# Kernel optimization log

Hardware: AMD Instinct MI355X
Metric: run time of the kernel (lower is better)

Reference implementation:

```python
import jax, jax.numpy as jnp
import numpy as np

A = 20.0  # sigmoid sharpness used by the module

def norm_sigmoid(x):
    # module's sigmoid: min/max normalize over the whole tensor, then steep sigmoid
    xn = (x - jnp.min(x)) / (jnp.max(x) - jnp.min(x))
    return jax.nn.sigmoid(A * xn)

def setup_inputs() -> dict:
    key = jax.random.key(0)
    ks = jax.random.split(key, 10)
    B, T = 2048, 512
    input_dim, nh1, nh2, nh3, output_dim = 1, 256, 256, 128, 1
    def lin(k, fan_in, fan_out):
        bound = 1.0 / np.sqrt(fan_in)
        kw, kb = jax.random.split(k)
        W = jax.random.uniform(kw, (fan_out, fan_in), jnp.float32, -bound, bound)
        b = jax.random.uniform(kb, (fan_out,), jnp.float32, -bound, bound)
        return W, b
    W1, b1 = lin(ks[0], input_dim, nh1)
    W2, b2 = lin(ks[1], nh1, nh2)
    W4, b4 = lin(ks[2], nh3, output_dim)
    j_w = jax.random.normal(ks[3], (nh3,), jnp.float32)
    k_w = jax.random.normal(ks[4], (nh3,), jnp.float32)
    X = jax.random.normal(ks[5], (B, T), jnp.float32)
    return {"X": X, "W1": W1, "b1": b1, "W2": W2, "b2": b2,
            "W4": W4, "b4": b4, "j_w": j_w, "k_w": k_w}

def reference(X, W1, b1, W2, b2, W4, b4, j_w, k_w):
    B, T = X.shape
    nh3 = j_w.shape[0]
    xs = jnp.swapaxes(X, 0, 1)[:, :, None]  # [T, B, 1] scalar input per step

    def step(state, x_t):
        out1 = norm_sigmoid(x_t @ W1.T + b1)          # [B, nh1]
        out2 = norm_sigmoid(out1 @ W2.T + b2)         # [B, nh2]
        j, k = out2[:, :nh3], out2[:, nh3:]
        inp_j = norm_sigmoid(j * j_w)
        inp_k = norm_sigmoid(k * k_w)
        new_state = (1.0 - state) * inp_j + (1.0 - inp_k) * state  # flip-flop update
        out4 = norm_sigmoid(new_state @ W4.T + b4)    # [B, 1]
        return new_state, out4

    state0 = jnp.zeros((B, nh3), X.dtype)
    _, ys = jax.lax.scan(step, state0, xs)            # ys: [T, B, 1]
    return jnp.squeeze(jnp.swapaxes(ys, 0, 1), axis=2)  # [B, T]
```

## Files before the change

### kernel.cpp

```cpp
#include <hip/hip_runtime.h>

#define TT 512
#define BB 2048
#define HH 256

typedef _Float16 f16x8 __attribute__((ext_vector_type(8)));
typedef _Float16 f16x4 __attribute__((ext_vector_type(4)));
typedef float f32x4 __attribute__((ext_vector_type(4)));

__device__ __forceinline__ float sigf(float z) { return 1.0f / (1.0f + __expf(-z)); }
__device__ __forceinline__ unsigned f2o(float f) {
    unsigned u = __float_as_uint(f);
    return (u & 0x80000000u) ? ~u : (u | 0x80000000u);
}
__device__ __forceinline__ float o2f(unsigned o) {
    unsigned u = (o & 0x80000000u) ? (o & 0x7fffffffu) : ~o;
    return __uint_as_float(u);
}

__global__ __launch_bounds__(256) void k0_stats(const float* __restrict__ X,
                                                const float* __restrict__ W1,
                                                const float* __restrict__ b1,
                                                float* __restrict__ mn1f, float* __restrict__ s1f,
                                                unsigned* __restrict__ colGmn,
                                                unsigned* __restrict__ colGmx,
                                                float2* __restrict__ statep) {
    int t = blockIdx.x, tid = threadIdx.x;
    statep[blockIdx.x * 256 + tid] = make_float2(0.f, 0.f);
    colGmn[(size_t)t * 256 + tid] = 0xFFFFFFFFu;
    colGmx[(size_t)t * 256 + tid] = 0u;
    __shared__ float rmn[256], rmx[256];
    float mn = 3.4e38f, mx = -3.4e38f;
    for (int b = tid; b < BB; b += 256) {
        float v = X[(size_t)b * TT + t];
        mn = fminf(mn, v); mx = fmaxf(mx, v);
    }
    rmn[tid] = mn; rmx[tid] = mx; __syncthreads();
    for (int s = 128; s > 0; s >>= 1) {
        if (tid < s) { rmn[tid] = fminf(rmn[tid], rmn[tid + s]); rmx[tid] = fmaxf(rmx[tid], rmx[tid + s]); }
        __syncthreads();
    }
    float xmn = rmn[0], xmx = rmx[0];
    __syncthreads();
    float w = W1[tid], bb = b1[tid];
    float v0 = w * xmn + bb, v1 = w * xmx + bb;
    rmn[tid] = fminf(v0, v1); rmx[tid] = fmaxf(v0, v1); __syncthreads();
    for (int s = 128; s > 0; s >>= 1) {
        if (tid < s) { rmn[tid] = fminf(rmn[tid], rmn[tid + s]); rmx[tid] = fmaxf(rmx[tid], rmx[tid + s]); }
        __syncthreads();
    }
    if (tid == 0) {
        mn1f[t] = rmn[0];
        s1f[t] = 20.0f / (rmx[0] - rmn[0]);
    }
}

__global__ __launch_bounds__(256) void k0b_cvt(const float* __restrict__ W2, _Float16* __restrict__ W2h) {
    int i4 = (blockIdx.x * 256 + threadIdx.x) * 4;
    float4 v = *(const float4*)&W2[i4];
    f16x4 h;
    h[0] = (_Float16)v.x; h[1] = (_Float16)v.y; h[2] = (_Float16)v.z; h[3] = (_Float16)v.w;
    *(f16x4*)&W2h[i4] = h;
}

__global__ __launch_bounds__(512) void k1_gemm(const float* __restrict__ X,
                                               const float* __restrict__ W1,
                                               const float* __restrict__ b1,
                                               const _Float16* __restrict__ W2h,
                                               const float* __restrict__ b2,
                                               const float* __restrict__ mn1f,
                                               const float* __restrict__ s1f,
                                               float* __restrict__ buf,
                                               unsigned* __restrict__ colGmn,
                                               unsigned* __restrict__ colGmx,
                                               int tbase) {
    int tl = blockIdx.z, t = tbase + tl;
    int bBase = blockIdx.x * 128;
    int tid = threadIdx.x;
    __shared__ __align__(16) _Float16 A_lds[128 * 72];
    __shared__ __align__(16) _Float16 B_lds[256 * 72];
    __shared__ float x_s[128];
    __shared__ unsigned cmnL[256], cmxL[256];
    if (tid < 128) x_s[tid] = X[(size_t)(bBase + tid) * TT + t];
    if (tid < 256) { cmnL[tid] = 0xFFFFFFFFu; cmxL[tid] = 0u; }
    float mn1 = mn1f[t], s1 = s1f[t];
    int lane = tid & 63, w = tid >> 6;
    int wr = w >> 2, wc = w & 3;
    int l15 = lane & 15, lk = (lane >> 4) * 8;
    f32x4 acc[4][4];
#pragma unroll
    for (int i = 0; i < 4; ++i)
#pragma unroll
        for (int j = 0; j < 4; ++j) acc[i][j] = (f32x4)0.0f;

    for (int kc = 0; kc < HH; kc += 64) {
        __syncthreads();
#pragma unroll
        for (int it = 0; it < 2; ++it) {
            int idx = it * 512 + tid;
            int row = idx >> 3, kg = (idx & 7) * 8;
            float x = x_s[row];
            float4 wa = *(const float4*)&W1[kc + kg];
            float4 wb = *(const float4*)&W1[kc + kg + 4];
            float4 ba = *(const float4*)&b1[kc + kg];
            float4 bb = *(const float4*)&b1[kc + kg + 4];
            f16x8 av;
            av[0] = (_Float16)sigf((x * wa.x + ba.x - mn1) * s1);
            av[1] = (_Float16)sigf((x * wa.y + ba.y - mn1) * s1);
            av[2] = (_Float16)sigf((x * wa.z + ba.z - mn1) * s1);
            av[3] = (_Float16)sigf((x * wa.w + ba.w - mn1) * s1);
            av[4] = (_Float16)sigf((x * wb.x + bb.x - mn1) * s1);
            av[5] = (_Float16)sigf((x * wb.y + bb.y - mn1) * s1);
            av[6] = (_Float16)sigf((x * wb.z + bb.z - mn1) * s1);
            av[7] = (_Float16)sigf((x * wb.w + bb.w - mn1) * s1);
            *(f16x8*)&A_lds[row * 72 + kg] = av;
        }
#pragma unroll
        for (int it = 0; it < 4; ++it) {
            int idx = it * 512 + tid;
            int c = idx >> 3, kg = (idx & 7) * 8;
            *(f16x8*)&B_lds[c * 72 + kg] = *(const f16x8*)&W2h[(size_t)c * HH + kc + kg];
        }
        __syncthreads();
#pragma unroll
        for (int ks = 0; ks < 64; ks += 32) {
            f16x8 af[4], bf[4];
#pragma unroll
            for (int i = 0; i < 4; ++i)
                af[i] = *(const f16x8*)&A_lds[(wr * 64 + i * 16 + l15) * 72 + ks + lk];
#pragma unroll
            for (int j = 0; j < 4; ++j)
                bf[j] = *(const f16x8*)&B_lds[(wc * 64 + j * 16 + l15) * 72 + ks + lk];
#pragma unroll
            for (int i = 0; i < 4; ++i)
#pragma unroll
                for (int j = 0; j < 4; ++j)
                    acc[i][j] = __builtin_amdgcn_mfma_f32_16x16x32_f16(af[i], bf[j], acc[i][j], 0, 0, 0);
        }
    }
#pragma unroll
    for (int j = 0; j < 4; ++j) {
        int c = wc * 64 + j * 16 + l15;
        float b2v = b2[c];
        float vmn = 3.4e38f, vmx = -3.4e38f;
#pragma unroll
        for (int i = 0; i < 4; ++i) {
            int r0 = wr * 64 + i * 16 + ((lane >> 4) << 2);
#pragma unroll
            for (int q = 0; q < 4; ++q) {
                float v = acc[i][j][q] + b2v;
                buf[((size_t)tl * BB + bBase + r0 + q) * HH + c] = v;
                vmn = fminf(vmn, v); vmx = fmaxf(vmx, v);
            }
        }
        atomicMin(&cmnL[c], f2o(vmn));
        atomicMax(&cmxL[c], f2o(vmx));
    }
    __syncthreads();
    if (tid < 256) {
        atomicMin(&colGmn[(size_t)t * 256 + tid], cmnL[tid]);
        atomicMax(&colGmx[(size_t)t * 256 + tid], cmxL[tid]);
    }
}

__global__ __launch_bounds__(256) void k1b(const unsigned* __restrict__ colGmn,
                                           const unsigned* __restrict__ colGmx,
                                           const float* __restrict__ j_w,
                                           const float* __restrict__ k_w,
                                           float* __restrict__ mn2f, float* __restrict__ s2f,
                                           float* __restrict__ mjf, float* __restrict__ sjf,
                                           float* __restrict__ mkf, float* __restrict__ skf,
                                           int tbase) {
    int t = tbase + blockIdx.x, tid = threadIdx.x;
    __shared__ float ra[256], rb[256];
    float cmn = o2f(colGmn[(size_t)t * 256 + tid]);
    float cmx = o2f(colGmx[(size_t)t * 256 + tid]);
    ra[tid] = cmn; rb[tid] = cmx; __syncthreads();
    for (int s = 128; s > 0; s >>= 1) {
        if (tid < s) { ra[tid] = fminf(ra[tid], ra[tid + s]); rb[tid] = fmaxf(rb[tid], rb[tid + s]); }
        __syncthreads();
    }
    float mn2 = ra[0], mx2 = rb[0];
    float s2 = 20.0f / (mx2 - mn2);
    __syncthreads();
    float lo = 3.4e38f, hi = -3.4e38f;
    if (tid < 128) {
        float wv = j_w[tid];
        float a = sigf((cmn - mn2) * s2) * wv;
        float b = sigf((cmx - mn2) * s2) * wv;
        lo = fminf(a, b); hi = fmaxf(a, b);
    }
    ra[tid] = lo; rb[tid] = hi; __syncthreads();
    for (int s = 128; s > 0; s >>= 1) {
        if (tid < s) { ra[tid] = fminf(ra[tid], ra[tid + s]); rb[tid] = fmaxf(rb[tid], rb[tid + s]); }
        __syncthreads();
    }
    float mj = ra[0], mxj = rb[0];
    __syncthreads();
    lo = 3.4e38f; hi = -3.4e38f;
    if (tid >= 128) {
        float wv = k_w[tid - 128];
        float a = sigf((cmn - mn2) * s2) * wv;
        float b = sigf((cmx - mn2) * s2) * wv;
        lo = fminf(a, b); hi = fmaxf(a, b);
    }
    ra[tid] = lo; rb[tid] = hi; __syncthreads();
    for (int s = 128; s > 0; s >>= 1) {
        if (tid < s) { ra[tid] = fminf(ra[tid], ra[tid + s]); rb[tid] = fmaxf(rb[tid], rb[tid + s]); }
        __syncthreads();
    }
    if (tid == 0) {
        mn2f[t] = mn2; s2f[t] = s2;
        mjf[t] = mj; sjf[t] = 20.0f / (ra[0] * 0.0f + rb[0] - mj);
    }
    if (tid == 0) {
        float mk = ra[0], mxk = rb[0];
        mkf[t] = mk; skf[t] = 20.0f / (mxk - mk);
        sjf[t] = 20.0f / (mxj - mj);
    }
}

__global__ __launch_bounds__(256) void k3_scan(const float* __restrict__ buf,
                                               const float* __restrict__ W4,
                                               const float* __restrict__ b4,
                                               const float* __restrict__ mn2f, const float* __restrict__ s2f,
                                               const float* __restrict__ mjf, const float* __restrict__ sjf,
                                               const float* __restrict__ mkf, const float* __restrict__ skf,
                                               const float* __restrict__ j_w, const float* __restrict__ k_w,
                                               float2* __restrict__ statep,
                                               float* __restrict__ out4p,
                                               int tbase, int TC) {
    __shared__ float n2L[512], c2L[512], mjL[512], sjL[512], mkL[512], skL[512];
    int tid = threadIdx.x;
    for (int tl = tid; tl < TC; tl += 256) {
        int t = tbase + tl;
        n2L[tl] = mn2f[t]; c2L[tl] = s2f[t];
        mjL[tl] = mjf[t]; sjL[tl] = sjf[t];
        mkL[tl] = mkf[t]; skL[tl] = skf[t];
    }
    __syncthreads();
    int wave = tid >> 6, lane = tid & 63;
    int b = blockIdx.x * 4 + wave;
    float w40 = W4[2 * lane], w41 = W4[2 * lane + 1];
    float jw0 = j_w[2 * lane], jw1 = j_w[2 * lane + 1];
    float kw0 = k_w[2 * lane], kw1 = k_w[2 * lane + 1];
    float bb4 = b4[0];
    float2 stv = statep[b * 64 + lane];
    float s0 = stv.x, s1v = stv.y;
    const float2* basep = (const float2*)buf;
    const int rowstride = BB * 128;
    int off0 = b * 128 + lane;
    float2 jq[8], kq[8];
#pragma unroll
    for (int u = 0; u < 8; ++u) {
        if (u < TC) {
            jq[u] = basep[(size_t)u * rowstride + off0];
            kq[u] = basep[(size_t)u * rowstride + off0 + 64];
        }
    }
    for (int t0 = 0; t0 < TC; t0 += 8) {
#pragma unroll
        for (int u = 0; u < 8; ++u) {
            int tl = t0 + u;
            if (tl >= TC) break;
            float2 jp = jq[u], kp = kq[u];
            int tn = tl + 8;
            if (tn < TC) {
                jq[u] = basep[(size_t)tn * rowstride + off0];
                kq[u] = basep[(size_t)tn * rowstride + off0 + 64];
            }
            float n2 = n2L[tl], c2 = c2L[tl];
            float pj0 = sigf((jp.x - n2) * c2) * jw0;
            float pj1 = sigf((jp.y - n2) * c2) * jw1;
            float pk0 = sigf((kp.x - n2) * c2) * kw0;
            float pk1 = sigf((kp.y - n2) * c2) * kw1;
            float ij0 = sigf((pj0 - mjL[tl]) * sjL[tl]);
            float ij1 = sigf((pj1 - mjL[tl]) * sjL[tl]);
            float ik0 = sigf((pk0 - mkL[tl]) * skL[tl]);
            float ik1 = sigf((pk1 - mkL[tl]) * skL[tl]);
            s0 = ij0 + s0 * (1.0f - ij0 - ik0);
            s1v = ij1 + s1v * (1.0f - ij1 - ik1);
            float r = s0 * w40 + s1v * w41;
#pragma unroll
            for (int m = 1; m < 64; m <<= 1) r += __shfl_xor(r, m);
            if (lane == 0) out4p[(size_t)b * TT + tbase + tl] = r + bb4;
        }
    }
    statep[b * 64 + lane] = make_float2(s0, s1v);
}

__global__ __launch_bounds__(256) void k3b(const float* __restrict__ out4p,
                                           float* __restrict__ mn4f, float* __restrict__ s4f) {
    int t = blockIdx.x, tid = threadIdx.x;
    __shared__ float rmn[256], rmx[256];
    float mn = 3.4e38f, mx = -3.4e38f;
    for (int b = tid; b < BB; b += 256) {
        float v = out4p[(size_t)b * TT + t];
        mn = fminf(mn, v); mx = fmaxf(mx, v);
    }
    rmn[tid] = mn; rmx[tid] = mx; __syncthreads();
    for (int s = 128; s > 0; s >>= 1) {
        if (tid < s) { rmn[tid] = fminf(rmn[tid], rmn[tid + s]); rmx[tid] = fmaxf(rmx[tid], rmx[tid + s]); }
        __syncthreads();
    }
    if (tid == 0) { mn4f[t] = rmn[0]; s4f[t] = 20.0f / (rmx[0] - rmn[0]); }
}

__global__ __launch_bounds__(256) void k4_final(float* __restrict__ out,
                                                const float* __restrict__ mn4f,
                                                const float* __restrict__ s4f) {
    int i = blockIdx.x * 256 + threadIdx.x;
    float4 v = ((const float4*)out)[i];
    int t0 = (i * 4) & (TT - 1);
    float4 mn = *(const float4*)&mn4f[t0];
    float4 sc = *(const float4*)&s4f[t0];
    float4 r;
    r.x = sigf((v.x - mn.x) * sc.x);
    r.y = sigf((v.y - mn.y) * sc.y);
    r.z = sigf((v.z - mn.z) * sc.z);
    r.w = sigf((v.w - mn.w) * sc.w);
    ((float4*)out)[i] = r;
}

extern "C" void kernel_launch(void* const* d_in, const int* in_sizes, int n_in,
                              void* d_out, int out_size, void* d_ws, size_t ws_size,
                              hipStream_t stream) {
    const float* X  = (const float*)d_in[0];
    const float* W1 = (const float*)d_in[1];
    const float* b1 = (const float*)d_in[2];
    const float* W2 = (const float*)d_in[3];
    const float* b2 = (const float*)d_in[4];
    const float* W4 = (const float*)d_in[5];
    const float* b4 = (const float*)d_in[6];
    const float* j_w = (const float*)d_in[7];
    const float* k_w = (const float*)d_in[8];
    float* out = (float*)d_out;

    const size_t stateB = (size_t)BB * 64 * sizeof(float2);
    const size_t colGB  = (size_t)TT * 256 * 2 * 4;
    const size_t w2hB   = (size_t)HH * HH * 2;
    const size_t statsB = 65536;
    int TC = 512;
    while (TC > 8 && ((size_t)TC * BB * HH * 4 + stateB + colGB + w2hB + statsB) > ws_size) TC >>= 1;
    int NC = TT / TC;

    char* w = (char*)d_ws;
    float* buf = (float*)w;
    size_t off = (size_t)TC * BB * HH * 4;
    float2* statep = (float2*)(w + off); off += stateB;
    unsigned* colGmn = (unsigned*)(w + off); off += colGB / 2;
    unsigned* colGmx = (unsigned*)(w + off); off += colGB / 2;
    _Float16* W2h = (_Float16*)(w + off); off += w2hB;
    float* fst = (float*)(w + off);
    float* mn1f = fst;        float* s1f = fst + 512;
    float* mn2f = fst + 1024; float* s2f = fst + 1536;
    float* mjf  = fst + 2048; float* sjf = fst + 2560;
    float* mkf  = fst + 3072; float* skf = fst + 3584;
    float* mn4f = fst + 4096; float* s4f = fst + 4608;
    float* out4p = out;

    k0_stats<<<512, 256, 0, stream>>>(X, W1, b1, mn1f, s1f, colGmn, colGmx, statep);
    k0b_cvt<<<64, 256, 0, stream>>>(W2, W2h);
    for (int c = 0; c < NC; ++c) {
        int tbase = c * TC;
        k1_gemm<<<dim3(BB / 128, 1, TC), 512, 0, stream>>>(X, W1, b1, W2h, b2, mn1f, s1f,
                                                           buf, colGmn, colGmx, tbase);
        k1b<<<TC, 256, 0, stream>>>(colGmn, colGmx, j_w, k_w, mn2f, s2f, mjf, sjf, mkf, skf, tbase);
        k3_scan<<<512, 256, 0, stream>>>(buf, W4, b4, mn2f, s2f, mjf, sjf, mkf, skf,
                                         j_w, k_w, statep, out4p, tbase, TC);
    }
    k3b<<<512, 256, 0, stream>>>(out4p, mn4f, s4f);
    k4_final<<<1024, 256, 0, stream>>>(out, mn4f, s4f);
}
```

Baseline: 916.6 us.

## Use split-fp16 three-MFMA GEMM with column-split tiles, LDS-staged stores, batched scan output

Splits both the layer-1 activations and W2 into fp16 high and low parts and issues three MFMAs per tile (lo*hi, hi*lo, hi*hi), which restores near-fp32 accuracy at roughly triple the matrix work. The GEMM grid now splits output columns across two blocks with a smaller K chunk, shrinking per-block tiles and LDS, and stages results through LDS so the stores to the global buffer are coalesced float4 writes. The column statistics are pre-reduced across lanes with shuffles before the atomics. The per-step j/k range reduction in k1b is merged into a single segmented pass, and the scan kernel buffers 64 outputs per lane and writes them in one coalesced store instead of a single-lane store every step.

```diff
diff --git a/kernel.cpp b/kernel.cpp
--- a/kernel.cpp
+++ b/kernel.cpp
@@ -3,6 +3,7 @@
 #define TT 512
 #define BB 2048
 #define HH 256
+#define KC 32
 
 typedef _Float16 f16x8 __attribute__((ext_vector_type(8)));
 typedef _Float16 f16x4 __attribute__((ext_vector_type(4)));
@@ -55,18 +56,26 @@
     }
 }
 
-__global__ __launch_bounds__(256) void k0b_cvt(const float* __restrict__ W2, _Float16* __restrict__ W2h) {
+__global__ __launch_bounds__(256) void k0b_cvt(const float* __restrict__ W2,
+                                               _Float16* __restrict__ W2hi,
+                                               _Float16* __restrict__ W2lo) {
     int i4 = (blockIdx.x * 256 + threadIdx.x) * 4;
     float4 v = *(const float4*)&W2[i4];
-    f16x4 h;
+    f16x4 h, l;
     h[0] = (_Float16)v.x; h[1] = (_Float16)v.y; h[2] = (_Float16)v.z; h[3] = (_Float16)v.w;
-    *(f16x4*)&W2h[i4] = h;
+    l[0] = (_Float16)(v.x - (float)h[0]);
+    l[1] = (_Float16)(v.y - (float)h[1]);
+    l[2] = (_Float16)(v.z - (float)h[2]);
+    l[3] = (_Float16)(v.w - (float)h[3]);
+    *(f16x4*)&W2hi[i4] = h;
+    *(f16x4*)&W2lo[i4] = l;
 }
 
 __global__ __launch_bounds__(512) void k1_gemm(const float* __restrict__ X,
                                                const float* __restrict__ W1,
                                                const float* __restrict__ b1,
-                                               const _Float16* __restrict__ W2h,
+                                               const _Float16* __restrict__ W2hi,
+                                               const _Float16* __restrict__ W2lo,
                                                const float* __restrict__ b2,
                                                const float* __restrict__ mn1f,
                                                const float* __restrict__ s1f,
@@ -76,90 +85,134 @@
                                                int tbase) {
     int tl = blockIdx.z, t = tbase + tl;
     int bBase = blockIdx.x * 128;
+    int cBase = blockIdx.y * 128;
     int tid = threadIdx.x;
-    __shared__ __align__(16) _Float16 A_lds[128 * 72];
-    __shared__ __align__(16) _Float16 B_lds[256 * 72];
-    __shared__ float x_s[128];
-    __shared__ unsigned cmnL[256], cmxL[256];
-    if (tid < 128) x_s[tid] = X[(size_t)(bBase + tid) * TT + t];
-    if (tid < 256) { cmnL[tid] = 0xFFFFFFFFu; cmxL[tid] = 0u; }
+    __shared__ __align__(16) char smem[42496];
+    _Float16* Ah = (_Float16*)smem;
+    _Float16* Al = Ah + 5120;
+    _Float16* Bh = Al + 5120;
+    _Float16* Bl = Bh + 5120;
+    float* C_lds = (float*)smem;
+    float* x_s = (float*)(smem + 40960);
+    unsigned* cmnL = (unsigned*)(smem + 41472);
+    unsigned* cmxL = cmnL + 128;
+    if (tid < 128) {
+        x_s[tid] = X[(size_t)(bBase + tid) * TT + t];
+        cmnL[tid] = 0xFFFFFFFFu; cmxL[tid] = 0u;
+    }
     float mn1 = mn1f[t], s1 = s1f[t];
     int lane = tid & 63, w = tid >> 6;
-    int wr = w >> 2, wc = w & 3;
-    int l15 = lane & 15, lk = (lane >> 4) * 8;
-    f32x4 acc[4][4];
-#pragma unroll
-    for (int i = 0; i < 4; ++i)
+    int wr = w & 3, wc = w >> 2;
+    int l15 = lane & 15, hi2 = lane >> 4, lk = hi2 * 8;
+    f32x4 acc[2][4];
+#pragma unroll
+    for (int i = 0; i < 2; ++i)
 #pragma unroll
         for (int j = 0; j < 4; ++j) acc[i][j] = (f32x4)0.0f;
 
-    for (int kc = 0; kc < HH; kc += 64) {
-        __syncthreads();
-#pragma unroll
-        for (int it = 0; it < 2; ++it) {
-            int idx = it * 512 + tid;
-            int row = idx >> 3, kg = (idx & 7) * 8;
-            float x = x_s[row];
-            float4 wa = *(const float4*)&W1[kc + kg];
-            float4 wb = *(const float4*)&W1[kc + kg + 4];
-            float4 ba = *(const float4*)&b1[kc + kg];
-            float4 bb = *(const float4*)&b1[kc + kg + 4];
-            f16x8 av;
-            av[0] = (_Float16)sigf((x * wa.x + ba.x - mn1) * s1);
-            av[1] = (_Float16)sigf((x * wa.y + ba.y - mn1) * s1);
-            av[2] = (_Float16)sigf((x * wa.z + ba.z - mn1) * s1);
-            av[3] = (_Float16)sigf((x * wa.w + ba.w - mn1) * s1);
-            av[4] = (_Float16)sigf((x * wb.x + bb.x - mn1) * s1);
-            av[5] = (_Float16)sigf((x * wb.y + bb.y - mn1) * s1);
-            av[6] = (_Float16)sigf((x * wb.z + bb.z - mn1) * s1);
-            av[7] = (_Float16)sigf((x * wb.w + bb.w - mn1) * s1);
-            *(f16x8*)&A_lds[row * 72 + kg] = av;
-        }
+    int sr = tid >> 2, skg = (tid & 3) * 8;
+    for (int kc = 0; kc < HH; kc += KC) {
+        __syncthreads();
+        {
+            float x = x_s[sr];
+            float4 wa = *(const float4*)&W1[kc + skg];
+            float4 wb = *(const float4*)&W1[kc + skg + 4];
+            float4 ba = *(const float4*)&b1[kc + skg];
+            float4 bb = *(const float4*)&b1[kc + skg + 4];
+            float a0 = sigf((x * wa.x + ba.x - mn1) * s1);
+            float a1 = sigf((x * wa.y + ba.y - mn1) * s1);
+            float a2 = sigf((x * wa.z + ba.z - mn1) * s1);
+            float a3 = sigf((x * wa.w + ba.w - mn1) * s1);
+            float a4 = sigf((x * wb.x + bb.x - mn1) * s1);
+            float a5 = sigf((x * wb.y + bb.y - mn1) * s1);
+            float a6 = sigf((x * wb.z + bb.z - mn1) * s1);
+            float a7 = sigf((x * wb.w + bb.w - mn1) * s1);
+            f16x8 hv, lv;
+            hv[0] = (_Float16)a0; lv[0] = (_Float16)(a0 - (float)hv[0]);
+            hv[1] = (_Float16)a1; lv[1] = (_Float16)(a1 - (float)hv[1]);
+            hv[2] = (_Float16)a2; lv[2] = (_Float16)(a2 - (float)hv[2]);
+            hv[3] = (_Float16)a3; lv[3] = (_Float16)(a3 - (float)hv[3]);
+            hv[4] = (_Float16)a4; lv[4] = (_Float16)(a4 - (float)hv[4]);
+            hv[5] = (_Float16)a5; lv[5] = (_Float16)(a5 - (float)hv[5]);
+            hv[6] = (_Float16)a6; lv[6] = (_Float16)(a6 - (float)hv[6]);
+            hv[7] = (_Float16)a7; lv[7] = (_Float16)(a7 - (float)hv[7]);
+            *(f16x8*)&Ah[sr * 40 + skg] = hv;
+            *(f16x8*)&Al[sr * 40 + skg] = lv;
+        }
+        {
+            size_t gsrc = (size_t)(cBase + sr) * HH + kc + skg;
+            *(f16x8*)&Bh[sr * 40 + skg] = *(const f16x8*)&W2hi[gsrc];
+            *(f16x8*)&Bl[sr * 40 + skg] = *(const f16x8*)&W2lo[gsrc];
+        }
+        __syncthreads();
+        f16x8 ah[2], alo[2], bh4[4], bl4[4];
+#pragma unroll
+        for (int i = 0; i < 2; ++i) {
+            int ro = (wr * 32 + i * 16 + l15) * 40 + lk;
+            ah[i] = *(const f16x8*)&Ah[ro];
+            alo[i] = *(const f16x8*)&Al[ro];
+        }
+#pragma unroll
+        for (int j = 0; j < 4; ++j) {
+            int co = (wc * 64 + j * 16 + l15) * 40 + lk;
+            bh4[j] = *(const f16x8*)&Bh[co];
+            bl4[j] = *(const f16x8*)&Bl[co];
+        }
+#pragma unroll
+        for (int i = 0; i < 2; ++i)
+#pragma unroll
+            for (int j = 0; j < 4; ++j) {
+                acc[i][j] = __builtin_amdgcn_mfma_f32_16x16x32_f16(alo[i], bh4[j], acc[i][j], 0, 0, 0);
+                acc[i][j] = __builtin_amdgcn_mfma_f32_16x16x32_f16(ah[i], bl4[j], acc[i][j], 0, 0, 0);
+                acc[i][j] = __builtin_amdgcn_mfma_f32_16x16x32_f16(ah[i], bh4[j], acc[i][j], 0, 0, 0);
+            }
+    }
+    float vout[2][4][4];
+#pragma unroll
+    for (int j = 0; j < 4; ++j) {
+        int cl = wc * 64 + j * 16 + l15;
+        float b2v = b2[cBase + cl];
+        float vmn = 3.4e38f, vmx = -3.4e38f;
+#pragma unroll
+        for (int i = 0; i < 2; ++i)
+#pragma unroll
+            for (int q = 0; q < 4; ++q) {
+                float v = acc[i][j][q] + b2v;
+                vout[i][j][q] = v;
+                vmn = fminf(vmn, v); vmx = fmaxf(vmx, v);
+            }
+        vmn = fminf(vmn, __shfl_xor(vmn, 16)); vmn = fminf(vmn, __shfl_xor(vmn, 32));
+        vmx = fmaxf(vmx, __shfl_xor(vmx, 16)); vmx = fmaxf(vmx, __shfl_xor(vmx, 32));
+        if (hi2 == 0) {
+            atomicMin(&cmnL[cl], f2o(vmn));
+            atomicMax(&cmxL[cl], f2o(vmx));
+        }
+    }
+    __syncthreads();
+#pragma unroll
+    for (int r = 0; r < 2; ++r) {
+        if (wc == r) {
+#pragma unroll
+            for (int i = 0; i < 2; ++i)
+#pragma unroll
+                for (int j = 0; j < 4; ++j)
+#pragma unroll
+                    for (int q = 0; q < 4; ++q)
+                        C_lds[(wr * 32 + i * 16 + hi2 * 4 + q) * 68 + j * 16 + l15] = vout[i][j][q];
+        }
+        __syncthreads();
 #pragma unroll
         for (int it = 0; it < 4; ++it) {
             int idx = it * 512 + tid;
-            int c = idx >> 3, kg = (idx & 7) * 8;
-            *(f16x8*)&B_lds[c * 72 + kg] = *(const f16x8*)&W2h[(size_t)c * HH + kc + kg];
-        }
-        __syncthreads();
-#pragma unroll
-        for (int ks = 0; ks < 64; ks += 32) {
-            f16x8 af[4], bf[4];
-#pragma unroll
-            for (int i = 0; i < 4; ++i)
-                af[i] = *(const f16x8*)&A_lds[(wr * 64 + i * 16 + l15) * 72 + ks + lk];
-#pragma unroll
-            for (int j = 0; j < 4; ++j)
-                bf[j] = *(const f16x8*)&B_lds[(wc * 64 + j * 16 + l15) * 72 + ks + lk];
-#pragma unroll
-            for (int i = 0; i < 4; ++i)
-#pragma unroll
-                for (int j = 0; j < 4; ++j)
-                    acc[i][j] = __builtin_amdgcn_mfma_f32_16x16x32_f16(af[i], bf[j], acc[i][j], 0, 0, 0);
-        }
-    }
-#pragma unroll
-    for (int j = 0; j < 4; ++j) {
-        int c = wc * 64 + j * 16 + l15;
-        float b2v = b2[c];
-        float vmn = 3.4e38f, vmx = -3.4e38f;
-#pragma unroll
-        for (int i = 0; i < 4; ++i) {
-            int r0 = wr * 64 + i * 16 + ((lane >> 4) << 2);
-#pragma unroll
-            for (int q = 0; q < 4; ++q) {
-                float v = acc[i][j][q] + b2v;
-                buf[((size_t)tl * BB + bBase + r0 + q) * HH + c] = v;
-                vmn = fminf(vmn, v); vmx = fmaxf(vmx, v);
-            }
-        }
-        atomicMin(&cmnL[c], f2o(vmn));
-        atomicMax(&cmxL[c], f2o(vmx));
-    }
-    __syncthreads();
-    if (tid < 256) {
-        atomicMin(&colGmn[(size_t)t * 256 + tid], cmnL[tid]);
-        atomicMax(&colGmx[(size_t)t * 256 + tid], cmxL[tid]);
+            int row = idx >> 4, c4 = idx & 15;
+            float4 v = *(const float4*)&C_lds[row * 68 + c4 * 4];
+            *(float4*)&buf[((size_t)tl * BB + bBase + row) * HH + cBase + r * 64 + c4 * 4] = v;
+        }
+        __syncthreads();
+    }
+    if (tid < 128) {
+        atomicMin(&colGmn[(size_t)t * 256 + cBase + tid], cmnL[tid]);
+        atomicMax(&colGmx[(size_t)t * 256 + cBase + tid], cmxL[tid]);
     }
 }
 
@@ -183,40 +236,20 @@
     float mn2 = ra[0], mx2 = rb[0];
     float s2 = 20.0f / (mx2 - mn2);
     __syncthreads();
-    float lo = 3.4e38f, hi = -3.4e38f;
-    if (tid < 128) {
-        float wv = j_w[tid];
-        float a = sigf((cmn - mn2) * s2) * wv;
-        float b = sigf((cmx - mn2) * s2) * wv;
-        lo = fminf(a, b); hi = fmaxf(a, b);
-    }
-    ra[tid] = lo; rb[tid] = hi; __syncthreads();
-    for (int s = 128; s > 0; s >>= 1) {
-        if (tid < s) { ra[tid] = fminf(ra[tid], ra[tid + s]); rb[tid] = fmaxf(rb[tid], rb[tid + s]); }
-        __syncthreads();
-    }
-    float mj = ra[0], mxj = rb[0];
-    __syncthreads();
-    lo = 3.4e38f; hi = -3.4e38f;
-    if (tid >= 128) {
-        float wv = k_w[tid - 128];
-        float a = sigf((cmn - mn2) * s2) * wv;
-        float b = sigf((cmx - mn2) * s2) * wv;
-        lo = fminf(a, b); hi = fmaxf(a, b);
-    }
-    ra[tid] = lo; rb[tid] = hi; __syncthreads();
-    for (int s = 128; s > 0; s >>= 1) {
-        if (tid < s) { ra[tid] = fminf(ra[tid], ra[tid + s]); rb[tid] = fmaxf(rb[tid], rb[tid + s]); }
+    float wv = (tid < 128) ? j_w[tid] : k_w[tid - 128];
+    float ea = sigf((cmn - mn2) * s2) * wv;
+    float eb = sigf((cmx - mn2) * s2) * wv;
+    ra[tid] = fminf(ea, eb); rb[tid] = fmaxf(ea, eb); __syncthreads();
+    for (int s = 64; s > 0; s >>= 1) {
+        if ((tid & 127) < s) { ra[tid] = fminf(ra[tid], ra[tid + s]); rb[tid] = fmaxf(rb[tid], rb[tid + s]); }
         __syncthreads();
     }
     if (tid == 0) {
         mn2f[t] = mn2; s2f[t] = s2;
-        mjf[t] = mj; sjf[t] = 20.0f / (ra[0] * 0.0f + rb[0] - mj);
-    }
-    if (tid == 0) {
-        float mk = ra[0], mxk = rb[0];
-        mkf[t] = mk; skf[t] = 20.0f / (mxk - mk);
-        sjf[t] = 20.0f / (mxj - mj);
+        mjf[t] = ra[0]; sjf[t] = 20.0f / (rb[0] - ra[0]);
+    }
+    if (tid == 128) {
+        mkf[t] = ra[128]; skf[t] = 20.0f / (rb[128] - ra[128]);
     }
 }
 
@@ -250,19 +283,17 @@
     const float2* basep = (const float2*)buf;
     const int rowstride = BB * 128;
     int off0 = b * 128 + lane;
+    float rsave = 0.f;
     float2 jq[8], kq[8];
 #pragma unroll
     for (int u = 0; u < 8; ++u) {
-        if (u < TC) {
-            jq[u] = basep[(size_t)u * rowstride + off0];
-            kq[u] = basep[(size_t)u * rowstride + off0 + 64];
-        }
+        jq[u] = basep[(size_t)u * rowstride + off0];
+        kq[u] = basep[(size_t)u * rowstride + off0 + 64];
     }
     for (int t0 = 0; t0 < TC; t0 += 8) {
 #pragma unroll
         for (int u = 0; u < 8; ++u) {
             int tl = t0 + u;
-            if (tl >= TC) break;
             float2 jp = jq[u], kp = kq[u];
             int tn = tl + 8;
             if (tn < TC) {
@@ -283,9 +314,14 @@
             float r = s0 * w40 + s1v * w41;
 #pragma unroll
             for (int m = 1; m < 64; m <<= 1) r += __shfl_xor(r, m);
-            if (lane == 0) out4p[(size_t)b * TT + tbase + tl] = r + bb4;
-        }
-    }
+            if (lane == (tl & 63)) rsave = r + bb4;
+        }
+        if (((t0 + 8) & 63) == 0) {
+            int base = t0 + 8 - 64;
+            out4p[(size_t)b * TT + tbase + base + lane] = rsave;
+        }
+    }
+    if (TC < 64 && lane < TC) out4p[(size_t)b * TT + tbase + lane] = rsave;
     statep[b * 64 + lane] = make_float2(s0, s1v);
 }
 
@@ -338,7 +374,7 @@
 
     const size_t stateB = (size_t)BB * 64 * sizeof(float2);
     const size_t colGB  = (size_t)TT * 256 * 2 * 4;
-    const size_t w2hB   = (size_t)HH * HH * 2;
+    const size_t w2hB   = (size_t)HH * HH * 2 * 2;
     const size_t statsB = 65536;
     int TC = 512;
     while (TC > 8 && ((size_t)TC * BB * HH * 4 + stateB + colGB + w2hB + statsB) > ws_size) TC >>= 1;
@@ -350,7 +386,8 @@
     float2* statep = (float2*)(w + off); off += stateB;
     unsigned* colGmn = (unsigned*)(w + off); off += colGB / 2;
     unsigned* colGmx = (unsigned*)(w + off); off += colGB / 2;
-    _Float16* W2h = (_Float16*)(w + off); off += w2hB;
+    _Float16* W2hi = (_Float16*)(w + off); off += w2hB / 2;
+    _Float16* W2lo = (_Float16*)(w + off); off += w2hB / 2;
     float* fst = (float*)(w + off);
     float* mn1f = fst;        float* s1f = fst + 512;
     float* mn2f = fst + 1024; float* s2f = fst + 1536;
@@ -360,10 +397,10 @@
     float* out4p = out;
 
     k0_stats<<<512, 256, 0, stream>>>(X, W1, b1, mn1f, s1f, colGmn, colGmx, statep);
-    k0b_cvt<<<64, 256, 0, stream>>>(W2, W2h);
+    k0b_cvt<<<64, 256, 0, stream>>>(W2, W2hi, W2lo);
     for (int c = 0; c < NC; ++c) {
         int tbase = c * TC;
-        k1_gemm<<<dim3(BB / 128, 1, TC), 512, 0, stream>>>(X, W1, b1, W2h, b2, mn1f, s1f,
+        k1_gemm<<<dim3(BB / 128, 2, TC), 512, 0, stream>>>(X, W1, b1, W2hi, W2lo, b2, mn1f, s1f,
                                                            buf, colGmn, colGmx, tbase);
         k1b<<<TC, 256, 0, stream>>>(colGmn, colGmx, j_w, k_w, mn2f, s2f, mjf, sjf, mkf, skf, tbase);
         k3_scan<<<512, 256, 0, stream>>>(buf, W4, b4, mn2f, s2f, mjf, sjf, mkf, skf,
```

Result: slower. 1.163 ms (+26.9%).
